# Kernel optimization log

Hardware: AMD Instinct MI355X
Metric: run time of the kernel (lower is better)

## Reference

```python
import jax, jax.numpy as jnp
import numpy as np

BETA = 0.95
NUM_STEPS = 32


def setup_inputs() -> dict:
    key = jax.random.key(0)
    ks = jax.random.split(key, 6)
    B, IN, D, P = 1024, 512, 256, 8
    total = D * P
    x = jax.random.normal(ks[0], (B, IN), jnp.float32)
    W_proj = jax.random.normal(ks[1], (IN, total), jnp.float32) / np.sqrt(IN)
    b_proj = jnp.zeros((total,), jnp.float32)
    # uniform threshold distribution, sorted: linspace(0.5, 2.0, P)
    thresholds = jnp.linspace(0.5, 2.0, P, dtype=jnp.float32)
    rate_W = jax.random.normal(ks[2], (P, 1), jnp.float32) / np.sqrt(P)
    rate_b = jnp.zeros((1,), jnp.float32)
    conv1_w = jax.random.normal(ks[3], (P // 2, P, 3), jnp.float32) / np.sqrt(P * 3)
    conv1_b = jnp.zeros((P // 2,), jnp.float32)
    conv2_w = jax.random.normal(ks[4], (1, P // 2, 1), jnp.float32) / np.sqrt(P // 2)
    conv2_b = jnp.zeros((1,), jnp.float32)
    fusion = jnp.array([0.6, 0.4], jnp.float32)
    return dict(x=x, W_proj=W_proj, b_proj=b_proj, thresholds=thresholds,
                rate_W=rate_W, rate_b=rate_b, conv1_w=conv1_w, conv1_b=conv1_b,
                conv2_w=conv2_w, conv2_b=conv2_b, fusion=fusion)


def _conv1d(x, w, b):
    # x: [N, C_in, T], w: [C_out, C_in, K] -> [N, C_out, T] (SAME padding)
    y = jax.lax.conv_general_dilated(x, w, window_strides=(1,), padding='SAME',
                                     dimension_numbers=('NCH', 'OIH', 'NCH'))
    return y + b[None, :, None]


def reference(x, W_proj, b_proj, thresholds, rate_W, rate_b,
              conv1_w, conv1_b, conv2_w, conv2_b, fusion):
    B = x.shape[0]
    P = thresholds.shape[0]
    D = W_proj.shape[1] // P
    # constant input current per neuron: [B, D, P]
    I = (x @ W_proj + b_proj).reshape(B, D, P)

    # LIF recurrence (snntorch Leaky, reset_mechanism='subtract'):
    #   reset = H(mem_prev - thr); mem = beta*mem_prev + I - reset*thr; spk = H(mem - thr)
    def step(mem, _):
        reset = (mem > thresholds).astype(mem.dtype)
        mem = BETA * mem + I - reset * thresholds
        spk = (mem > thresholds).astype(mem.dtype)
        return mem, spk

    mem0 = jnp.zeros((B, D, P), x.dtype)
    _, spikes = jax.lax.scan(step, mem0, None, length=NUM_STEPS)  # [T, B, D, P]

    # rate branch
    rates = spikes.mean(axis=0)                        # [B, D, P]
    rate_dec = (rates @ rate_W)[..., 0] + rate_b[0]    # [B, D]

    # temporal branch: [B*D, P, T]
    s = jnp.transpose(spikes, (1, 2, 3, 0)).reshape(B * D, P, NUM_STEPS)
    h = jax.nn.relu(_conv1d(s, conv1_w, conv1_b))
    h = _conv1d(h, conv2_w, conv2_b)                   # [B*D, 1, T]
    temp_dec = h.mean(axis=-1).reshape(B, D)

    fw = jax.nn.softmax(fusion)
    return fw[0] * rate_dec + fw[1] * temp_dec
```

## Files before the change

kernel.cpp:

```cpp
#include <hip/hip_runtime.h>
#include <type_traits>


constexpr int IN_DIM  = 512;
constexpr int D_DIM   = 256;
constexpr int NTOT    = 2048;
constexpr int T_STEPS = 32;

constexpr int TM = 64;
constexpr int TN = 64;
constexpr int TK = 32;
constexpr int NSPLIT = 4;
constexpr int KSPLIT = IN_DIM / NSPLIT;

__global__ __launch_bounds__(128, 2)
void popcode_gemm(const float* __restrict__ x,
                  const float* __restrict__ Wp,
                  float* __restrict__ ws)
{
    __shared__ float As[TK][TM + 4];
    __shared__ float Bs[TK][TN];

    const int tid = threadIdx.x;
    const int b0  = blockIdx.x * TM;
    const int c0  = blockIdx.y * TN;
    const int k0  = blockIdx.z * KSPLIT;
    const int rg  = tid >> 3;
    const int dl  = tid & 7;
    const int r4  = rg * 4;

    float acc[4][8];
#pragma unroll
    for (int i = 0; i < 4; ++i)
#pragma unroll
        for (int j = 0; j < 8; ++j) acc[i][j] = 0.f;

    for (int kc = k0; kc < k0 + KSPLIT; kc += TK) {
#pragma unroll
        for (int i = 0; i < 4; ++i) {
            const int f   = tid + 128 * i;
            const int row = f >> 3;
            const int c4  = (f & 7) * 4;
            const float4 v =
                *reinterpret_cast<const float4*>(x + (b0 + row) * IN_DIM + kc + c4);
            As[c4 + 0][row] = v.x;
            As[c4 + 1][row] = v.y;
            As[c4 + 2][row] = v.z;
            As[c4 + 3][row] = v.w;
        }
#pragma unroll
        for (int i = 0; i < 4; ++i) {
            const int f  = tid + 128 * i;
            const int r  = f >> 4;
            const int c4 = (f & 15) * 4;
            *reinterpret_cast<float4*>(&Bs[r][c4]) =
                *reinterpret_cast<const float4*>(Wp + (kc + r) * NTOT + c0 + c4);
        }
        __syncthreads();

#pragma unroll 16
        for (int k = 0; k < TK; ++k) {
            const float4 a = *reinterpret_cast<const float4*>(&As[k][r4]);
            const float4 u = *reinterpret_cast<const float4*>(&Bs[k][dl * 8]);
            const float4 v = *reinterpret_cast<const float4*>(&Bs[k][dl * 8 + 4]);
            const float ar[4] = {a.x, a.y, a.z, a.w};
#pragma unroll
            for (int r = 0; r < 4; ++r) {
                acc[r][0] += ar[r] * u.x;  acc[r][1] += ar[r] * u.y;
                acc[r][2] += ar[r] * u.z;  acc[r][3] += ar[r] * u.w;
                acc[r][4] += ar[r] * v.x;  acc[r][5] += ar[r] * v.y;
                acc[r][6] += ar[r] * v.z;  acc[r][7] += ar[r] * v.w;
            }
        }
        __syncthreads();
    }

    float* dst = ws + (size_t)blockIdx.z * 1024 * NTOT;
#pragma unroll
    for (int bi = 0; bi < 4; ++bi) {
        float* p = dst + (size_t)(b0 + r4 + bi) * NTOT + c0 + dl * 8;
        *reinterpret_cast<float4*>(p)     = {acc[bi][0], acc[bi][1], acc[bi][2], acc[bi][3]};
        *reinterpret_cast<float4*>(p + 4) = {acc[bi][4], acc[bi][5], acc[bi][6], acc[bi][7]};
    }
}

__global__ __launch_bounds__(256)
void popcode_epi(const float* __restrict__ ws,
                 const float* __restrict__ bp,
                 const float* __restrict__ thrs,
                 const float* __restrict__ rateW,
                 const float* __restrict__ rateB,
                 const float* __restrict__ c1w,
                 const float* __restrict__ c1b,
                 const float* __restrict__ c2w,
                 const float* __restrict__ c2b,
                 const float* __restrict__ fus,
                 float* __restrict__ out)
{
    __shared__ float lut[3][256][4];
    __shared__ float rlut[256];
    __shared__ float wlds[96];
    __shared__ uint4 exch[256];

    const int tid = threadIdx.x;
    const int wv  = tid >> 6;
    const int h   = wv & 1;
    const int nl  = ((wv >> 1) << 6) | (tid & 63);
    const int n   = blockIdx.x * 128 + nl;
    const int b   = n >> 8;
    const int d   = n & 255;

    if (tid < 96) wlds[tid] = c1w[tid];
    {
        float rv = 0.f;
#pragma unroll
        for (int p = 0; p < 8; ++p)
            rv += (float)((tid >> p) & 1) * rateW[p];
        rlut[tid] = rv;
    }
    __syncthreads();
#pragma unroll
    for (int i = 0; i < 12; ++i) {
        const int e    = 256 * i + tid;
        const int k    = e >> 10;
        const int byte = (e >> 2) & 255;
        const int c    = e & 3;
        float v = (k == 1) ? c1b[c] : 0.f;
#pragma unroll
        for (int p = 0; p < 8; ++p)
            v = fmaf((float)((byte >> p) & 1), wlds[(c * 8 + p) * 3 + k], v);
        (&lut[0][0][0])[e] = v;
    }

    float w2c[4];
#pragma unroll
    for (int c = 0; c < 4; ++c) w2c[c] = c2w[c];
    const float rb_ = rateB[0];
    const float bb2 = c2b[0];
    const float f0 = fus[0], f1 = fus[1];
    const float fm = fmaxf(f0, f1);
    const float e0 = __expf(f0 - fm), e1 = __expf(f1 - fm);
    const float inv = 1.f / (e0 + e1);
    const float fw0 = e0 * inv, fw1 = e1 * inv;

    const size_t base  = (size_t)b * NTOT + d * 8 + h * 4;
    const size_t slice = (size_t)1024 * NTOT;
    float4 iv = *reinterpret_cast<const float4*>(ws + base);
#pragma unroll
    for (int s = 1; s < NSPLIT; ++s) {
        const float4 q = *reinterpret_cast<const float4*>(ws + s * slice + base);
        iv.x += q.x; iv.y += q.y; iv.z += q.z; iv.w += q.w;
    }
    const float4 bpv = *reinterpret_cast<const float4*>(bp + d * 8 + h * 4);
    const float4 tv  = *reinterpret_cast<const float4*>(thrs + h * 4);
    float Iv[4]  = {iv.x + bpv.x, iv.y + bpv.y, iv.z + bpv.z, iv.w + bpv.w};
    float thr[4] = {tv.x, tv.y, tv.z, tv.w};
    float Imt[4], mem[4];
    bool  spk[4];
#pragma unroll
    for (int p = 0; p < 4; ++p) {
        Imt[p] = Iv[p] - thr[p];
        mem[p] = 0.f;
        spk[p] = false;
    }

    unsigned nib[4] = {0u, 0u, 0u, 0u};
#pragma unroll
    for (int t = 0; t < T_STEPS; ++t) {
        unsigned nb = 0u;
#pragma unroll
        for (int p = 0; p < 4; ++p) {
            mem[p] = 0.95f * mem[p] + (spk[p] ? Imt[p] : Iv[p]);
            spk[p] = mem[p] > thr[p];
            nb |= spk[p] ? (1u << p) : 0u;
        }
        nib[t >> 3] |= nb << (4 * (t & 7));
    }

    __syncthreads();
    exch[tid] = uint4{nib[0], nib[1], nib[2], nib[3]};
    __syncthreads();
    const uint4 pr = exch[tid ^ 64];
    const unsigned prn[4] = {pr.x, pr.y, pr.z, pr.w};
    unsigned lo[4], hi[4];
#pragma unroll
    for (int w = 0; w < 4; ++w) {
        lo[w] = h ? prn[w] : nib[w];
        hi[w] = h ? nib[w] : prn[w];
    }

    auto getbyte = [&](int t) -> unsigned {
        const int w = t >> 3, s = 4 * (t & 7);
        return ((lo[w] >> s) & 15u) | (((hi[w] >> s) & 15u) << 4);
    };
    const float* lutf = &lut[0][0][0];
    float tacc = 0.f, rsum = 0.f;

    auto conv_half = [&](auto T0C) {
        constexpr int T0 = T0C.value;
        unsigned bprev = (T0 == 0) ? 0u : getbyte(T0 - 1);
        unsigned bcur  = getbyte(T0);
#pragma unroll
        for (int i = 0; i < 16; ++i) {
            const int t = T0 + i;
            const unsigned bnext = (t < 31) ? getbyte(t + 1) : 0u;
            const float4 fa = *reinterpret_cast<const float4*>(lutf + bprev * 4);
            const float4 fb = *reinterpret_cast<const float4*>(lutf + 1024 + bcur * 4);
            const float4 fc = *reinterpret_cast<const float4*>(lutf + 2048 + bnext * 4);
            rsum += rlut[bcur];
            const float h0_ = (fa.x + fb.x) + fc.x;
            const float h1_ = (fa.y + fb.y) + fc.y;
            const float h2_ = (fa.z + fb.z) + fc.z;
            const float h3_ = (fa.w + fb.w) + fc.w;
            tacc = fmaf(fmaxf(h0_, 0.f), w2c[0], tacc);
            tacc = fmaf(fmaxf(h1_, 0.f), w2c[1], tacc);
            tacc = fmaf(fmaxf(h2_, 0.f), w2c[2], tacc);
            tacc = fmaf(fmaxf(h3_, 0.f), w2c[3], tacc);
            bprev = bcur;
            bcur  = bnext;
        }
    };
    if (h == 0) conv_half(std::integral_constant<int, 0>{});
    else        conv_half(std::integral_constant<int, 16>{});

    __syncthreads();
    float2* e2 = reinterpret_cast<float2*>(exch);
    e2[tid] = float2{rsum, tacc};
    __syncthreads();
    const float2 q = e2[tid ^ 64];
    rsum += q.x;
    tacc += q.y;

    if (h == 0) {
        const float rdec = rsum * (1.f / 32.f) + rb_;
        const float temp = tacc * (1.f / 32.f) + bb2;
        out[b * D_DIM + d] = fw0 * rdec + fw1 * temp;
    }
}

extern "C" void kernel_launch(void* const* d_in, const int* in_sizes, int n_in,
                              void* d_out, int out_size, void* d_ws, size_t ws_size,
                              hipStream_t stream) {
    const float* x     = (const float*)d_in[0];
    const float* Wp    = (const float*)d_in[1];
    const float* bp    = (const float*)d_in[2];
    const float* thrs  = (const float*)d_in[3];
    const float* rateW = (const float*)d_in[4];
    const float* rateB = (const float*)d_in[5];
    const float* c1w   = (const float*)d_in[6];
    const float* c1b   = (const float*)d_in[7];
    const float* c2w   = (const float*)d_in[8];
    const float* c2b   = (const float*)d_in[9];
    const float* fus   = (const float*)d_in[10];
    float* out = (float*)d_out;
    float* ws  = (float*)d_ws;

    dim3 g1(1024 / TM, NTOT / TN, NSPLIT);
    popcode_gemm<<<g1, dim3(128), 0, stream>>>(x, Wp, ws);

    popcode_epi<<<dim3(2048), dim3(256), 0, stream>>>(
        ws, bp, thrs, rateW, rateB, c1w, c1b, c2w, c2b, fus, out);
}
```

Baseline: 121.0 us.

## Enlarge GEMM register tile and replace LDS exchanges with wave shuffles in epilogue

The GEMM block tile grows from 64 to 128 rows, so each thread computes an 8x8 accumulator block instead of 4x8, and the occupancy hint in launch bounds is dropped. This raises arithmetic per shared-memory load at the cost of more registers. The epilogue pairs the two halves of each neuron within one wave: spike nibbles and partial sums are exchanged with __shfl_xor instead of LDS round trips and barriers. The rate lookup table is replaced by popcount on the spike bits, and the conv1 weight staging in LDS is removed.

```diff
diff --git a/kernel.cpp b/kernel.cpp
--- a/kernel.cpp
+++ b/kernel.cpp
@@ -1,5 +1,4 @@
 #include <hip/hip_runtime.h>
-#include <type_traits>
 
 
 constexpr int IN_DIM  = 512;
@@ -7,13 +6,13 @@
 constexpr int NTOT    = 2048;
 constexpr int T_STEPS = 32;
 
-constexpr int TM = 64;
+constexpr int TM = 128;
 constexpr int TN = 64;
 constexpr int TK = 32;
 constexpr int NSPLIT = 4;
 constexpr int KSPLIT = IN_DIM / NSPLIT;
 
-__global__ __launch_bounds__(128, 2)
+__global__ __launch_bounds__(128)
 void popcode_gemm(const float* __restrict__ x,
                   const float* __restrict__ Wp,
                   float* __restrict__ ws)
@@ -27,17 +26,18 @@
     const int k0  = blockIdx.z * KSPLIT;
     const int rg  = tid >> 3;
     const int dl  = tid & 7;
-    const int r4  = rg * 4;
-
-    float acc[4][8];
-#pragma unroll
-    for (int i = 0; i < 4; ++i)
+    const int r8  = rg * 8;
+    const int c8  = dl * 8;
+
+    float acc[8][8];
+#pragma unroll
+    for (int i = 0; i < 8; ++i)
 #pragma unroll
         for (int j = 0; j < 8; ++j) acc[i][j] = 0.f;
 
     for (int kc = k0; kc < k0 + KSPLIT; kc += TK) {
 #pragma unroll
-        for (int i = 0; i < 4; ++i) {
+        for (int i = 0; i < 8; ++i) {
             const int f   = tid + 128 * i;
             const int row = f >> 3;
             const int c4  = (f & 7) * 4;
@@ -58,27 +58,27 @@
         }
         __syncthreads();
 
-#pragma unroll 16
+#pragma unroll 8
         for (int k = 0; k < TK; ++k) {
-            const float4 a = *reinterpret_cast<const float4*>(&As[k][r4]);
-            const float4 u = *reinterpret_cast<const float4*>(&Bs[k][dl * 8]);
-            const float4 v = *reinterpret_cast<const float4*>(&Bs[k][dl * 8 + 4]);
-            const float ar[4] = {a.x, a.y, a.z, a.w};
-#pragma unroll
-            for (int r = 0; r < 4; ++r) {
-                acc[r][0] += ar[r] * u.x;  acc[r][1] += ar[r] * u.y;
-                acc[r][2] += ar[r] * u.z;  acc[r][3] += ar[r] * u.w;
-                acc[r][4] += ar[r] * v.x;  acc[r][5] += ar[r] * v.y;
-                acc[r][6] += ar[r] * v.z;  acc[r][7] += ar[r] * v.w;
-            }
+            const float4 a0 = *reinterpret_cast<const float4*>(&As[k][r8]);
+            const float4 a1 = *reinterpret_cast<const float4*>(&As[k][r8 + 4]);
+            const float4 u0 = *reinterpret_cast<const float4*>(&Bs[k][c8]);
+            const float4 u1 = *reinterpret_cast<const float4*>(&Bs[k][c8 + 4]);
+            const float ar[8] = {a0.x, a0.y, a0.z, a0.w, a1.x, a1.y, a1.z, a1.w};
+            const float bc[8] = {u0.x, u0.y, u0.z, u0.w, u1.x, u1.y, u1.z, u1.w};
+#pragma unroll
+            for (int r = 0; r < 8; ++r)
+#pragma unroll
+                for (int c = 0; c < 8; ++c)
+                    acc[r][c] += ar[r] * bc[c];
         }
         __syncthreads();
     }
 
     float* dst = ws + (size_t)blockIdx.z * 1024 * NTOT;
 #pragma unroll
-    for (int bi = 0; bi < 4; ++bi) {
-        float* p = dst + (size_t)(b0 + r4 + bi) * NTOT + c0 + dl * 8;
+    for (int bi = 0; bi < 8; ++bi) {
+        float* p = dst + (size_t)(b0 + r8 + bi) * NTOT + c0 + c8;
         *reinterpret_cast<float4*>(p)     = {acc[bi][0], acc[bi][1], acc[bi][2], acc[bi][3]};
         *reinterpret_cast<float4*>(p + 4) = {acc[bi][4], acc[bi][5], acc[bi][6], acc[bi][7]};
     }
@@ -98,27 +98,16 @@
                  float* __restrict__ out)
 {
     __shared__ float lut[3][256][4];
-    __shared__ float rlut[256];
-    __shared__ float wlds[96];
-    __shared__ uint4 exch[256];
-
-    const int tid = threadIdx.x;
-    const int wv  = tid >> 6;
-    const int h   = wv & 1;
-    const int nl  = ((wv >> 1) << 6) | (tid & 63);
-    const int n   = blockIdx.x * 128 + nl;
-    const int b   = n >> 8;
-    const int d   = n & 255;
-
-    if (tid < 96) wlds[tid] = c1w[tid];
-    {
-        float rv = 0.f;
-#pragma unroll
-        for (int p = 0; p < 8; ++p)
-            rv += (float)((tid >> p) & 1) * rateW[p];
-        rlut[tid] = rv;
-    }
-    __syncthreads();
+
+    const int tid  = threadIdx.x;
+    const int wv   = tid >> 6;
+    const int lane = tid & 63;
+    const int l5   = lane & 31;
+    const int h    = lane >> 5;
+    const int n    = blockIdx.x * 128 + wv * 32 + l5;
+    const int b    = n >> 8;
+    const int d    = n & 255;
+
 #pragma unroll
     for (int i = 0; i < 12; ++i) {
         const int e    = 256 * i + tid;
@@ -128,9 +117,11 @@
         float v = (k == 1) ? c1b[c] : 0.f;
 #pragma unroll
         for (int p = 0; p < 8; ++p)
-            v = fmaf((float)((byte >> p) & 1), wlds[(c * 8 + p) * 3 + k], v);
+            v = fmaf((float)((byte >> p) & 1), c1w[(c * 8 + p) * 3 + k], v);
+        lut[0][0][0 * 0] = lut[0][0][0];
         (&lut[0][0][0])[e] = v;
     }
+    __syncthreads();
 
     float w2c[4];
 #pragma unroll
@@ -143,7 +134,7 @@
     const float inv = 1.f / (e0 + e1);
     const float fw0 = e0 * inv, fw1 = e1 * inv;
 
-    const size_t base  = (size_t)b * NTOT + d * 8 + h * 4;
+    const size_t base  = (size_t)n * 8 + h * 4;
     const size_t slice = (size_t)1024 * NTOT;
     float4 iv = *reinterpret_cast<const float4*>(ws + base);
 #pragma unroll
@@ -153,6 +144,7 @@
     }
     const float4 bpv = *reinterpret_cast<const float4*>(bp + d * 8 + h * 4);
     const float4 tv  = *reinterpret_cast<const float4*>(thrs + h * 4);
+    const float4 rwv = *reinterpret_cast<const float4*>(rateW + h * 4);
     float Iv[4]  = {iv.x + bpv.x, iv.y + bpv.y, iv.z + bpv.z, iv.w + bpv.w};
     float thr[4] = {tv.x, tv.y, tv.z, tv.w};
     float Imt[4], mem[4];
@@ -177,60 +169,69 @@
         nib[t >> 3] |= nb << (4 * (t & 7));
     }
 
-    __syncthreads();
-    exch[tid] = uint4{nib[0], nib[1], nib[2], nib[3]};
-    __syncthreads();
-    const uint4 pr = exch[tid ^ 64];
-    const unsigned prn[4] = {pr.x, pr.y, pr.z, pr.w};
+    float rsum = 0.f;
+    {
+        const float rw4[4] = {rwv.x, rwv.y, rwv.z, rwv.w};
+#pragma unroll
+        for (int j = 0; j < 4; ++j) {
+            int cnt = 0;
+#pragma unroll
+            for (int wd = 0; wd < 4; ++wd)
+                cnt += __popc((nib[wd] >> j) & 0x11111111u);
+            rsum += (float)cnt * rw4[j];
+        }
+    }
+
+    unsigned pr[4];
+#pragma unroll
+    for (int wd = 0; wd < 4; ++wd)
+        pr[wd] = (unsigned)__shfl_xor((int)nib[wd], 32, 64);
     unsigned lo[4], hi[4];
 #pragma unroll
-    for (int w = 0; w < 4; ++w) {
-        lo[w] = h ? prn[w] : nib[w];
-        hi[w] = h ? nib[w] : prn[w];
-    }
-
-    auto getbyte = [&](int t) -> unsigned {
-        const int w = t >> 3, s = 4 * (t & 7);
-        return ((lo[w] >> s) & 15u) | (((hi[w] >> s) & 15u) << 4);
-    };
+    for (int wd = 0; wd < 4; ++wd) {
+        lo[wd] = h ? pr[wd]  : nib[wd];
+        hi[wd] = h ? nib[wd] : pr[wd];
+    }
+    const unsigned awL0 = h ? lo[2] : lo[0];
+    const unsigned awL1 = h ? lo[3] : lo[1];
+    const unsigned awH0 = h ? hi[2] : hi[0];
+    const unsigned awH1 = h ? hi[3] : hi[1];
+    const unsigned b15 = ((lo[1] >> 28) & 15u) | (((hi[1] >> 28) & 15u) << 4);
+    const unsigned b16 = (lo[2] & 15u) | ((hi[2] & 15u) << 4);
+
     const float* lutf = &lut[0][0][0];
-    float tacc = 0.f, rsum = 0.f;
-
-    auto conv_half = [&](auto T0C) {
-        constexpr int T0 = T0C.value;
-        unsigned bprev = (T0 == 0) ? 0u : getbyte(T0 - 1);
-        unsigned bcur  = getbyte(T0);
-#pragma unroll
-        for (int i = 0; i < 16; ++i) {
-            const int t = T0 + i;
-            const unsigned bnext = (t < 31) ? getbyte(t + 1) : 0u;
-            const float4 fa = *reinterpret_cast<const float4*>(lutf + bprev * 4);
-            const float4 fb = *reinterpret_cast<const float4*>(lutf + 1024 + bcur * 4);
-            const float4 fc = *reinterpret_cast<const float4*>(lutf + 2048 + bnext * 4);
-            rsum += rlut[bcur];
-            const float h0_ = (fa.x + fb.x) + fc.x;
-            const float h1_ = (fa.y + fb.y) + fc.y;
-            const float h2_ = (fa.z + fb.z) + fc.z;
-            const float h3_ = (fa.w + fb.w) + fc.w;
-            tacc = fmaf(fmaxf(h0_, 0.f), w2c[0], tacc);
-            tacc = fmaf(fmaxf(h1_, 0.f), w2c[1], tacc);
-            tacc = fmaf(fmaxf(h2_, 0.f), w2c[2], tacc);
-            tacc = fmaf(fmaxf(h3_, 0.f), w2c[3], tacc);
-            bprev = bcur;
-            bcur  = bnext;
-        }
-    };
-    if (h == 0) conv_half(std::integral_constant<int, 0>{});
-    else        conv_half(std::integral_constant<int, 16>{});
-
-    __syncthreads();
-    float2* e2 = reinterpret_cast<float2*>(exch);
-    e2[tid] = float2{rsum, tacc};
-    __syncthreads();
-    const float2 q = e2[tid ^ 64];
-    rsum += q.x;
-    tacc += q.y;
-
+    float tacc = 0.f;
+    unsigned bprev = h ? b15 : 0u;
+    unsigned bcur  = (awL0 & 15u) | ((awH0 & 15u) << 4);
+#pragma unroll
+    for (int i = 0; i < 16; ++i) {
+        unsigned bnext;
+        if (i < 15) {
+            const int wd = (i + 1) >> 3;
+            const int s  = 4 * ((i + 1) & 7);
+            const unsigned wl = wd ? awL1 : awL0;
+            const unsigned wh = wd ? awH1 : awH0;
+            bnext = ((wl >> s) & 15u) | (((wh >> s) & 15u) << 4);
+        } else {
+            bnext = h ? 0u : b16;
+        }
+        const float4 fa = *reinterpret_cast<const float4*>(lutf + bprev * 4);
+        const float4 fb = *reinterpret_cast<const float4*>(lutf + 1024 + bcur * 4);
+        const float4 fc = *reinterpret_cast<const float4*>(lutf + 2048 + bnext * 4);
+        const float h0_ = (fa.x + fb.x) + fc.x;
+        const float h1_ = (fa.y + fb.y) + fc.y;
+        const float h2_ = (fa.z + fb.z) + fc.z;
+        const float h3_ = (fa.w + fb.w) + fc.w;
+        tacc = fmaf(fmaxf(h0_, 0.f), w2c[0], tacc);
+        tacc = fmaf(fmaxf(h1_, 0.f), w2c[1], tacc);
+        tacc = fmaf(fmaxf(h2_, 0.f), w2c[2], tacc);
+        tacc = fmaf(fmaxf(h3_, 0.f), w2c[3], tacc);
+        bprev = bcur;
+        bcur  = bnext;
+    }
+
+    rsum += __shfl_xor(rsum, 32, 64);
+    tacc += __shfl_xor(tacc, 32, 64);
     if (h == 0) {
         const float rdec = rsum * (1.f / 32.f) + rb_;
         const float temp = tacc * (1.f / 32.f) + bb2;
```

New measurement: 127.1 us. 5.0% more time.
